# Performance work log

Measured on AMD Instinct MI355X. Metric: run time of the kernel, lower is better.

Reference implementation:

```python
import jax, jax.numpy as jnp
import numpy as np

# Instant-NGP style multiresolution hash grid config
L = 16                      # n_levels
F = 2                       # n_feat_per_entry
LEVEL_SIZE = 524288         # 2^19 hash entries per level
RES = np.array([16, 22, 30, 42, 58, 80, 111, 154, 212, 294, 406, 561, 776, 1072, 1482, 2048], np.int32)
OFFSETS = (np.arange(L + 1) * LEVEL_SIZE).astype(np.int32)
PRIMES = np.array([1, 2654435761, 805459861], dtype=np.uint32)  # spatial hash primes
# 8 corner offsets of a voxel, (8, 3) in {0,1}
CORNERS = np.array([[(c >> d) & 1 for d in range(3)] for c in range(8)], np.int32)


def setup_inputs() -> dict:
    key = jax.random.key(0)
    k1, k2 = jax.random.split(key)
    B = 1000000
    xyz = jax.random.uniform(k1, (B, 3), dtype=jnp.float32)  # points in [0,1)
    embeddings = jax.random.normal(k2, (int(OFFSETS[-1]), F), dtype=jnp.float32) * 0.01
    return {
        'xyz': xyz,
        'embeddings': embeddings,
        'min_xyz': jnp.zeros((3,), jnp.float32),
        'max_xyz': jnp.ones((3,), jnp.float32),
    }


def _encode(xyz, embeddings, min_xyz, max_xyz):
    B = xyz.shape[0]
    norm = (xyz - min_xyz) / (max_xyz - min_xyz)          # (B, 3) in [0,1] if inside grid
    valid = jnp.all((norm >= 0.0) & (norm <= 1.0), axis=-1)  # (B,)
    corners = jnp.asarray(CORNERS)                        # (8, 3)
    primes = jnp.asarray(PRIMES)
    outs = []
    for l in range(L):  # fixed small loop over levels (different resolution per level)
        r = int(RES[l])
        pos = norm * (r - 1)                              # (B, 3) grid coords
        fi = jnp.clip(jnp.floor(pos).astype(jnp.int32), 0, r - 2)  # (B, 3) base corner
        frac = pos - fi.astype(pos.dtype)                 # (B, 3) trilinear fraction
        c = fi[:, None, :] + corners[None, :, :]          # (B, 8, 3) corner coords
        # trilinear interpolation weights, (B, 8)
        w = jnp.prod(jnp.where(corners[None] == 1, frac[:, None, :], 1.0 - frac[:, None, :]), axis=-1)
        # spatial hash into this level's table slice
        cu = c.astype(jnp.uint32)
        h = (cu[..., 0] * primes[0]) ^ (cu[..., 1] * primes[1]) ^ (cu[..., 2] * primes[2])
        lvl_size = jnp.uint32(int(OFFSETS[l + 1] - OFFSETS[l]))
        idx = (h % lvl_size).astype(jnp.int32) + int(OFFSETS[l])   # (B, 8) global entry ids
        feats = embeddings[idx]                           # (B, 8, F) irregular gather
        outs.append(jnp.sum(w[..., None] * feats, axis=1))  # (B, F)
    out = jnp.stack(outs, axis=1).reshape(B, L * F)       # (B, L*F)
    return jnp.where(valid[:, None], out, jnp.zeros((), out.dtype))


def reference(xyz, embeddings, min_xyz, max_xyz):
    return _encode(xyz, embeddings, min_xyz, max_xyz)
```

## Files before the change

### kernel.cpp

```cpp
#include <hip/hip_runtime.h>
#include <hip/hip_fp16.h>
#include <stdint.h>

#define NLEVELS 16
#define BLOCK 256
#define NPT 2

#define P1 2654435761u
#define P2 805459861u
#define HMASK 0x7FFFFu

__device__ __host__ constexpr int DRES(int l) {
    constexpr int r[6] = {16, 22, 30, 42, 58, 80};
    return r[l];
}
__device__ __host__ constexpr uint32_t DOFF(int l) {
    constexpr uint32_t o[6] = {0, 4096, 14744, 41744, 115832, 310944};
    return o[l];
}
#define DENSE_ENTRIES 822944u
#define HASH16_ENTRIES (10u << 19)
#define HASH16_BYTES ((size_t)HASH16_ENTRIES * 4)
#define DENSE_BYTES  ((size_t)DENSE_ENTRIES * 4)


__global__ __launch_bounds__(BLOCK) void convert_hash_kernel(
    const float* __restrict__ emb, uint32_t* __restrict__ tab16)
{
    const uint32_t i = blockIdx.x * BLOCK + threadIdx.x;
    if (i >= HASH16_ENTRIES) return;
    const float2 v = *reinterpret_cast<const float2*>(
        emb + (((size_t)(6u << 19)) + i) * 2);
    __half2 hv = __floats2half2_rn(v.x, v.y);
    __builtin_nontemporal_store(*reinterpret_cast<uint32_t*>(&hv), &tab16[i]);
}

template <int LIDX>
__global__ __launch_bounds__(BLOCK) void dense_build_kernel(
    const float* __restrict__ emb, uint32_t* __restrict__ dense)
{
    constexpr int r = DRES(LIDX);
    constexpr uint32_t off = DOFF(LIDX);
    const int n = r * r * r;
    const int i = blockIdx.x * BLOCK + threadIdx.x;
    if (i >= n) return;
    const int z = i / (r * r);
    const int rem = i - z * (r * r);
    const int y = rem / r;
    const int x = rem - y * r;
    const uint32_t h = ((uint32_t)x ^ ((uint32_t)y * P1) ^ ((uint32_t)z * P2)) & HMASK;
    const float2 v = *reinterpret_cast<const float2*>(
        emb + (((size_t)LIDX << 19) + h) * 2);
    __half2 hv = __floats2half2_rn(v.x, v.y);
    dense[off + i] = *reinterpret_cast<uint32_t*>(&hv);
}


struct PointCtx { float nx, ny, nz; bool valid; };

__device__ __forceinline__ PointCtx make_ctx(const float* __restrict__ xyz, int pt, int B,
                                             float mn0, float mn1, float mn2,
                                             float inv0, float inv1, float inv2)
{
    PointCtx P;
    P.nx = P.ny = P.nz = 0.0f;
    P.valid = false;
    if (pt < B) {
        const float x = xyz[3 * pt + 0];
        const float y = xyz[3 * pt + 1];
        const float z = xyz[3 * pt + 2];
        P.nx = (x - mn0) * inv0;
        P.ny = (y - mn1) * inv1;
        P.nz = (z - mn2) * inv2;
        P.valid = (P.nx >= 0.0f) && (P.nx <= 1.0f) &&
                  (P.ny >= 0.0f) && (P.ny <= 1.0f) &&
                  (P.nz >= 0.0f) && (P.nz <= 1.0f);
    }
    return P;
}

struct C8 { uint32_t idx[8]; float w[8]; };

__device__ __forceinline__ void frac_setup(const PointCtx& P, int r,
                                           int& fx, int& fy, int& fz,
                                           float& wx0, float& wx1,
                                           float& wy0, float& wy1,
                                           float& wz0, float& wz1)
{
    const float rm1 = (float)(r - 1);
    const float px = P.nx * rm1, py = P.ny * rm1, pz = P.nz * rm1;
    fx = (int)floorf(px); fx = min(max(fx, 0), r - 2);
    fy = (int)floorf(py); fy = min(max(fy, 0), r - 2);
    fz = (int)floorf(pz); fz = min(max(fz, 0), r - 2);
    wx1 = px - (float)fx; wx0 = 1.0f - wx1;
    wy1 = py - (float)fy; wy0 = 1.0f - wy1;
    wz1 = pz - (float)fz; wz0 = 1.0f - wz1;
}

__device__ __forceinline__ C8 mk_hash(const PointCtx& P, int r)
{
    int fx, fy, fz; float wx0, wx1, wy0, wy1, wz0, wz1;
    frac_setup(P, r, fx, fy, fz, wx0, wx1, wy0, wy1, wz0, wz1);
    const uint32_t hx0 = (uint32_t)fx,        hx1 = hx0 + 1u;
    const uint32_t hy0 = (uint32_t)fy * P1,   hy1 = hy0 + P1;
    const uint32_t hz0 = (uint32_t)fz * P2,   hz1 = hz0 + P2;
    C8 c;
    #pragma unroll
    for (int k = 0; k < 8; ++k) {
        c.idx[k] = (((k & 1) ? hx1 : hx0) ^
                    ((k & 2) ? hy1 : hy0) ^
                    ((k & 4) ? hz1 : hz0)) & HMASK;
        c.w[k] = ((k & 1) ? wx1 : wx0) * ((k & 2) ? wy1 : wy0) * ((k & 4) ? wz1 : wz0);
    }
    return c;
}

__device__ __forceinline__ C8 mk_dense(const PointCtx& P, int r, uint32_t off)
{
    int fx, fy, fz; float wx0, wx1, wy0, wy1, wz0, wz1;
    frac_setup(P, r, fx, fy, fz, wx0, wx1, wy0, wy1, wz0, wz1);
    const uint32_t base = off + (uint32_t)(fx + fy * r + fz * r * r);
    C8 c;
    #pragma unroll
    for (int k = 0; k < 8; ++k) {
        c.idx[k] = base + (uint32_t)((k & 1) + ((k & 2) ? r : 0) + ((k & 4) ? r * r : 0));
        c.w[k] = ((k & 1) ? wx1 : wx0) * ((k & 2) ? wy1 : wy0) * ((k & 4) ? wz1 : wz0);
    }
    return c;
}

__device__ __forceinline__ float2 accum8(const C8& c, const uint32_t* e, bool valid)
{
    float a = 0.0f, b = 0.0f;
    #pragma unroll
    for (int k = 0; k < 8; ++k) {
        const float2 f = __half22float2(*reinterpret_cast<const __half2*>(&e[k]));
        a = fmaf(c.w[k], f.x, a);
        b = fmaf(c.w[k], f.y, b);
    }
    float2 o;
    o.x = valid ? a : 0.0f;
    o.y = valid ? b : 0.0f;
    return o;
}

__device__ __forceinline__ void nt_store_f2h(uint32_t* p, float2 v)
{
    __half2 h = __floats2half2_rn(v.x, v.y);
    __builtin_nontemporal_store(*reinterpret_cast<uint32_t*>(&h), p);
}

__global__ __launch_bounds__(BLOCK, 4) void dense_low_kernel(
    const float* __restrict__ xyz,
    const uint32_t* __restrict__ dense,
    const float* __restrict__ minv,
    const float* __restrict__ maxv,
    uint32_t* __restrict__ slab,
    int B)
{
    const int t = threadIdx.x;
    const int p0 = blockIdx.x * (NPT * BLOCK) + t;
    const int p1 = p0 + BLOCK;

    const float mn0 = minv[0], mn1 = minv[1], mn2 = minv[2];
    const float inv0 = 1.0f / (maxv[0] - mn0);
    const float inv1 = 1.0f / (maxv[1] - mn1);
    const float inv2 = 1.0f / (maxv[2] - mn2);

    const PointCtx A = make_ctx(xyz, p0, B, mn0, mn1, mn2, inv0, inv1, inv2);
    const PointCtx Bc = make_ctx(xyz, p1, B, mn0, mn1, mn2, inv0, inv1, inv2);

    #pragma unroll
    for (int l = 0; l < 5; ++l) {
        const C8 c0 = mk_dense(A,  DRES(l), DOFF(l));
        const C8 c1 = mk_dense(Bc, DRES(l), DOFF(l));
        uint32_t e0[8], e1[8];
        #pragma unroll
        for (int k = 0; k < 8; ++k) e0[k] = dense[c0.idx[k]];
        #pragma unroll
        for (int k = 0; k < 8; ++k) e1[k] = dense[c1.idx[k]];
        const float2 o0 = accum8(c0, e0, A.valid);
        const float2 o1 = accum8(c1, e1, Bc.valid);
        if (p0 < B) nt_store_f2h(&slab[(size_t)l * B + p0], o0);
        if (p1 < B) nt_store_f2h(&slab[(size_t)l * B + p1], o1);
    }
}

__global__ __launch_bounds__(BLOCK, 4) void dense_l5_kernel(
    const float* __restrict__ xyz,
    const uint32_t* __restrict__ dense,
    const float* __restrict__ minv,
    const float* __restrict__ maxv,
    uint32_t* __restrict__ slab,
    int B)
{
    const int t = threadIdx.x;
    const int p0 = blockIdx.x * (NPT * BLOCK) + t;
    const int p1 = p0 + BLOCK;

    const float mn0 = minv[0], mn1 = minv[1], mn2 = minv[2];
    const float inv0 = 1.0f / (maxv[0] - mn0);
    const float inv1 = 1.0f / (maxv[1] - mn1);
    const float inv2 = 1.0f / (maxv[2] - mn2);

    const PointCtx A = make_ctx(xyz, p0, B, mn0, mn1, mn2, inv0, inv1, inv2);
    const PointCtx Bc = make_ctx(xyz, p1, B, mn0, mn1, mn2, inv0, inv1, inv2);

    const C8 c0 = mk_dense(A,  DRES(5), DOFF(5));
    const C8 c1 = mk_dense(Bc, DRES(5), DOFF(5));
    uint32_t e0[8], e1[8];
    #pragma unroll
    for (int k = 0; k < 8; ++k) e0[k] = dense[c0.idx[k]];
    #pragma unroll
    for (int k = 0; k < 8; ++k) e1[k] = dense[c1.idx[k]];
    __builtin_amdgcn_sched_barrier(0);
    const float2 o0 = accum8(c0, e0, A.valid);
    const float2 o1 = accum8(c1, e1, Bc.valid);
    if (p0 < B) nt_store_f2h(&slab[(size_t)5 * B + p0], o0);
    if (p1 < B) nt_store_f2h(&slab[(size_t)5 * B + p1], o1);
}

template <int L, int R>
__global__ __launch_bounds__(BLOCK, 4) void hash_level_kernel(
    const float* __restrict__ xyz,
    const uint32_t* __restrict__ tab16,
    const float* __restrict__ minv,
    const float* __restrict__ maxv,
    uint32_t* __restrict__ slab,
    int B)
{
    const uint32_t* __restrict__ lt = tab16 + ((size_t)(L - 6) << 19);
    const int t = threadIdx.x;
    const int p0 = blockIdx.x * (NPT * BLOCK) + t;
    const int p1 = p0 + BLOCK;

    const float mn0 = minv[0], mn1 = minv[1], mn2 = minv[2];
    const float inv0 = 1.0f / (maxv[0] - mn0);
    const float inv1 = 1.0f / (maxv[1] - mn1);
    const float inv2 = 1.0f / (maxv[2] - mn2);

    const PointCtx A = make_ctx(xyz, p0, B, mn0, mn1, mn2, inv0, inv1, inv2);
    const PointCtx Bc = make_ctx(xyz, p1, B, mn0, mn1, mn2, inv0, inv1, inv2);

    const C8 c0 = mk_hash(A,  R);
    const C8 c1 = mk_hash(Bc, R);
    uint32_t e0[8], e1[8];
    #pragma unroll
    for (int k = 0; k < 8; ++k) e0[k] = lt[c0.idx[k]];
    #pragma unroll
    for (int k = 0; k < 8; ++k) e1[k] = lt[c1.idx[k]];
    __builtin_amdgcn_sched_barrier(0);
    const float2 o0 = accum8(c0, e0, A.valid);
    const float2 o1 = accum8(c1, e1, Bc.valid);
    if (p0 < B) nt_store_f2h(&slab[(size_t)L * B + p0], o0);
    if (p1 < B) nt_store_f2h(&slab[(size_t)L * B + p1], o1);
}

__global__ __launch_bounds__(BLOCK) void transpose_kernel(
    const uint32_t* __restrict__ slab,
    float* __restrict__ out,
    int B)
{
    __shared__ float s[32][BLOCK + 1];
    const int t = threadIdx.x;
    const int pt = blockIdx.x * BLOCK + t;

    #pragma unroll
    for (int l = 0; l < NLEVELS; ++l) {
        float2 v = make_float2(0.0f, 0.0f);
        if (pt < B) {
            const uint32_t bits = __builtin_nontemporal_load(&slab[(size_t)l * B + pt]);
            v = __half22float2(*reinterpret_cast<const __half2*>(&bits));
        }
        s[2 * l + 0][t] = v.x;
        s[2 * l + 1][t] = v.y;
    }
    __syncthreads();

    const size_t chunk = (size_t)blockIdx.x * (BLOCK * 32);
    const size_t total = (size_t)B * 32;
    #pragma unroll
    for (int k = 0; k < 32; ++k) {
        const int flat = k * BLOCK + t;
        const int p = flat >> 5;
        const int c = flat & 31;
        const size_t g = chunk + (size_t)flat;
        if (g < total) __builtin_nontemporal_store(s[c][p], &out[g]);
    }
}

__global__ __launch_bounds__(BLOCK) void hashgrid_fused_kernel(
    const float* __restrict__ xyz,
    const float* __restrict__ emb,
    const float* __restrict__ minv,
    const float* __restrict__ maxv,
    float* __restrict__ out,
    int B)
{
    constexpr int RES[NLEVELS] = {16, 22, 30, 42, 58, 80, 111, 154,
                                  212, 294, 406, 561, 776, 1072, 1482, 2048};
    __shared__ float s[32][BLOCK + 1];
    const int t = threadIdx.x;
    const int pt = blockIdx.x * BLOCK + t;

    const float mn0 = minv[0], mn1 = minv[1], mn2 = minv[2];
    const float inv0 = 1.0f / (maxv[0] - mn0);
    const float inv1 = 1.0f / (maxv[1] - mn1);
    const float inv2 = 1.0f / (maxv[2] - mn2);

    const PointCtx P = make_ctx(xyz, pt, B, mn0, mn1, mn2, inv0, inv1, inv2);

    #pragma unroll
    for (int l = 0; l < NLEVELS; ++l) {
        const C8 c = mk_hash(P, RES[l]);
        const float* __restrict__ lemb = emb + ((size_t)l << 20);
        float acc0 = 0.0f, acc1 = 0.0f;
        #pragma unroll
        for (int k = 0; k < 8; ++k) {
            const float2 f = *reinterpret_cast<const float2*>(
                lemb + ((size_t)c.idx[k] << 1));
            acc0 = fmaf(c.w[k], f.x, acc0);
            acc1 = fmaf(c.w[k], f.y, acc1);
        }
        s[2 * l + 0][t] = P.valid ? acc0 : 0.0f;
        s[2 * l + 1][t] = P.valid ? acc1 : 0.0f;
    }
    __syncthreads();
    const size_t chunk = (size_t)blockIdx.x * (BLOCK * 32);
    const size_t total = (size_t)B * 32;
    #pragma unroll
    for (int k = 0; k < 32; ++k) {
        const int flat = k * BLOCK + t;
        const int p = flat >> 5;
        const int c = flat & 31;
        const size_t g = chunk + (size_t)flat;
        if (g < total) out[g] = s[c][p];
    }
}

extern "C" void kernel_launch(void* const* d_in, const int* in_sizes, int n_in,
                              void* d_out, int out_size, void* d_ws, size_t ws_size,
                              hipStream_t stream) {
    const float* xyz = (const float*)d_in[0];
    const float* emb = (const float*)d_in[1];
    const float* mn  = (const float*)d_in[2];
    const float* mx  = (const float*)d_in[3];
    float* out = (float*)d_out;

    const int B = in_sizes[0] / 3;
    const int blocks1 = (B + BLOCK - 1) / BLOCK;
    const int blocks2 = (B + NPT * BLOCK - 1) / (NPT * BLOCK);

    const size_t slab_bytes = (size_t)NLEVELS * (size_t)B * 4;
    const size_t ws_needed = slab_bytes + HASH16_BYTES + DENSE_BYTES;

    if (ws_size >= ws_needed) {
        uint32_t* slab  = (uint32_t*)d_ws;
        uint32_t* tab16 = (uint32_t*)((char*)d_ws + slab_bytes);
        uint32_t* dense = (uint32_t*)((char*)d_ws + slab_bytes + HASH16_BYTES);

        hipLaunchKernelGGL(convert_hash_kernel,
                           dim3((HASH16_ENTRIES + BLOCK - 1) / BLOCK), dim3(BLOCK),
                           0, stream, emb, tab16);
        #define DBUILD(L) hipLaunchKernelGGL((dense_build_kernel<L>), \
            dim3((DRES(L)*DRES(L)*DRES(L) + BLOCK - 1) / BLOCK), dim3(BLOCK), 0, stream, emb, dense)
        DBUILD(0); DBUILD(1); DBUILD(2); DBUILD(3); DBUILD(4); DBUILD(5);
        #undef DBUILD

        hipLaunchKernelGGL(dense_low_kernel, dim3(blocks2), dim3(BLOCK), 0, stream,
                           xyz, dense, mn, mx, slab, B);
        hipLaunchKernelGGL(dense_l5_kernel, dim3(blocks2), dim3(BLOCK), 0, stream,
                           xyz, dense, mn, mx, slab, B);
        #define HLVL(L, R) hipLaunchKernelGGL((hash_level_kernel<L, R>), dim3(blocks2), dim3(BLOCK), 0, stream, xyz, tab16, mn, mx, slab, B)
        HLVL(6, 111);  HLVL(7, 154);  HLVL(8, 212);  HLVL(9, 294);
        HLVL(10, 406); HLVL(11, 561); HLVL(12, 776); HLVL(13, 1072);
        HLVL(14, 1482); HLVL(15, 2048);
        #undef HLVL

        hipLaunchKernelGGL(transpose_kernel, dim3(blocks1), dim3(BLOCK), 0, stream,
                           slab, out, B);
    } else {
        hipLaunchKernelGGL(hashgrid_fused_kernel, dim3(blocks1), dim3(BLOCK), 0, stream,
                           xyz, emb, mn, mx, out, B);
    }
}
```

Measured before the change: 387.6 us.

## Merge table prep and per-level gather kernels into two launches

Folds the hash-table fp16 conversion and the six dense-table builds into one prep kernel. All per-level gather kernels become a single mega kernel whose block index selects the level segment. This removes many kernel launches and the launch gaps and tail drains between them. In exchange the resolution becomes a runtime value in the hash segments, with runtime divides and branching, and the sched_barrier hints are dropped.

```diff
diff --git a/kernel.cpp b/kernel.cpp
--- a/kernel.cpp
+++ b/kernel.cpp
@@ -15,44 +15,43 @@
     return r[l];
 }
 __device__ __host__ constexpr uint32_t DOFF(int l) {
-    constexpr uint32_t o[6] = {0, 4096, 14744, 41744, 115832, 310944};
+    constexpr uint32_t o[7] = {0, 4096, 14744, 41744, 115832, 310944, 822944};
     return o[l];
 }
 #define DENSE_ENTRIES 822944u
 #define HASH16_ENTRIES (10u << 19)
 #define HASH16_BYTES ((size_t)HASH16_ENTRIES * 4)
 #define DENSE_BYTES  ((size_t)DENSE_ENTRIES * 4)
-
-
-__global__ __launch_bounds__(BLOCK) void convert_hash_kernel(
-    const float* __restrict__ emb, uint32_t* __restrict__ tab16)
+#define PREP_TOTAL   (HASH16_ENTRIES + DENSE_ENTRIES)
+
+__global__ __launch_bounds__(BLOCK) void prep_kernel(
+    const float* __restrict__ emb,
+    uint32_t* __restrict__ tab16,
+    uint32_t* __restrict__ dense)
 {
     const uint32_t i = blockIdx.x * BLOCK + threadIdx.x;
-    if (i >= HASH16_ENTRIES) return;
-    const float2 v = *reinterpret_cast<const float2*>(
-        emb + (((size_t)(6u << 19)) + i) * 2);
-    __half2 hv = __floats2half2_rn(v.x, v.y);
-    __builtin_nontemporal_store(*reinterpret_cast<uint32_t*>(&hv), &tab16[i]);
-}
-
-template <int LIDX>
-__global__ __launch_bounds__(BLOCK) void dense_build_kernel(
-    const float* __restrict__ emb, uint32_t* __restrict__ dense)
-{
-    constexpr int r = DRES(LIDX);
-    constexpr uint32_t off = DOFF(LIDX);
-    const int n = r * r * r;
-    const int i = blockIdx.x * BLOCK + threadIdx.x;
-    if (i >= n) return;
-    const int z = i / (r * r);
-    const int rem = i - z * (r * r);
-    const int y = rem / r;
-    const int x = rem - y * r;
-    const uint32_t h = ((uint32_t)x ^ ((uint32_t)y * P1) ^ ((uint32_t)z * P2)) & HMASK;
-    const float2 v = *reinterpret_cast<const float2*>(
-        emb + (((size_t)LIDX << 19) + h) * 2);
-    __half2 hv = __floats2half2_rn(v.x, v.y);
-    dense[off + i] = *reinterpret_cast<uint32_t*>(&hv);
+    if (i < HASH16_ENTRIES) {
+        const float2 v = *reinterpret_cast<const float2*>(
+            emb + (((size_t)(6u << 19)) + i) * 2);
+        __half2 hv = __floats2half2_rn(v.x, v.y);
+        __builtin_nontemporal_store(*reinterpret_cast<uint32_t*>(&hv), &tab16[i]);
+    } else if (i < PREP_TOTAL) {
+        const uint32_t j = i - HASH16_ENTRIES;
+        int l = 0;
+        #pragma unroll
+        for (int q = 1; q < 6; ++q) if (j >= DOFF(q)) l = q;
+        const int r = DRES(l);
+        const uint32_t rel = j - DOFF(l);
+        const int z = rel / (uint32_t)(r * r);
+        const uint32_t rem = rel - (uint32_t)z * (uint32_t)(r * r);
+        const int y = rem / (uint32_t)r;
+        const int x = rem - (uint32_t)y * (uint32_t)r;
+        const uint32_t h = ((uint32_t)x ^ ((uint32_t)y * P1) ^ ((uint32_t)z * P2)) & HMASK;
+        const float2 v = *reinterpret_cast<const float2*>(
+            emb + (((size_t)l << 19) + h) * 2);
+        __half2 hv = __floats2half2_rn(v.x, v.y);
+        dense[j] = *reinterpret_cast<uint32_t*>(&hv);
+    }
 }
 
 
@@ -150,16 +149,22 @@
     __builtin_nontemporal_store(*reinterpret_cast<uint32_t*>(&h), p);
 }
 
-__global__ __launch_bounds__(BLOCK, 4) void dense_low_kernel(
+__global__ __launch_bounds__(BLOCK, 4) void gather_mega_kernel(
     const float* __restrict__ xyz,
+    const uint32_t* __restrict__ tab16,
     const uint32_t* __restrict__ dense,
     const float* __restrict__ minv,
     const float* __restrict__ maxv,
     uint32_t* __restrict__ slab,
-    int B)
-{
+    int B, int blocks2)
+{
+    constexpr int HRES[10] = {111, 154, 212, 294, 406, 561, 776, 1072, 1482, 2048};
+
+    const int seg = blockIdx.x / blocks2;
+    const int blk = blockIdx.x - seg * blocks2;
+
     const int t = threadIdx.x;
-    const int p0 = blockIdx.x * (NPT * BLOCK) + t;
+    const int p0 = blk * (NPT * BLOCK) + t;
     const int p1 = p0 + BLOCK;
 
     const float mn0 = minv[0], mn1 = minv[1], mn2 = minv[2];
@@ -167,93 +172,52 @@
     const float inv1 = 1.0f / (maxv[1] - mn1);
     const float inv2 = 1.0f / (maxv[2] - mn2);
 
-    const PointCtx A = make_ctx(xyz, p0, B, mn0, mn1, mn2, inv0, inv1, inv2);
+    const PointCtx A  = make_ctx(xyz, p0, B, mn0, mn1, mn2, inv0, inv1, inv2);
     const PointCtx Bc = make_ctx(xyz, p1, B, mn0, mn1, mn2, inv0, inv1, inv2);
 
-    #pragma unroll
-    for (int l = 0; l < 5; ++l) {
-        const C8 c0 = mk_dense(A,  DRES(l), DOFF(l));
-        const C8 c1 = mk_dense(Bc, DRES(l), DOFF(l));
+    if (seg == 0) {
+        #pragma unroll
+        for (int l = 0; l < 5; ++l) {
+            const C8 c0 = mk_dense(A,  DRES(l), DOFF(l));
+            const C8 c1 = mk_dense(Bc, DRES(l), DOFF(l));
+            uint32_t e0[8], e1[8];
+            #pragma unroll
+            for (int k = 0; k < 8; ++k) e0[k] = dense[c0.idx[k]];
+            #pragma unroll
+            for (int k = 0; k < 8; ++k) e1[k] = dense[c1.idx[k]];
+            const float2 o0 = accum8(c0, e0, A.valid);
+            const float2 o1 = accum8(c1, e1, Bc.valid);
+            if (p0 < B) nt_store_f2h(&slab[(size_t)l * B + p0], o0);
+            if (p1 < B) nt_store_f2h(&slab[(size_t)l * B + p1], o1);
+        }
+    } else if (seg == 1) {
+        const C8 c0 = mk_dense(A,  DRES(5), DOFF(5));
+        const C8 c1 = mk_dense(Bc, DRES(5), DOFF(5));
         uint32_t e0[8], e1[8];
         #pragma unroll
         for (int k = 0; k < 8; ++k) e0[k] = dense[c0.idx[k]];
         #pragma unroll
         for (int k = 0; k < 8; ++k) e1[k] = dense[c1.idx[k]];
+        const float2 o0 = accum8(c0, e0, A.valid);
+        const float2 o1 = accum8(c1, e1, Bc.valid);
+        if (p0 < B) nt_store_f2h(&slab[(size_t)5 * B + p0], o0);
+        if (p1 < B) nt_store_f2h(&slab[(size_t)5 * B + p1], o1);
+    } else {
+        const int l = seg + 4;
+        const int r = HRES[seg - 2];
+        const uint32_t* __restrict__ lt = tab16 + ((size_t)(l - 6) << 19);
+        const C8 c0 = mk_hash(A,  r);
+        const C8 c1 = mk_hash(Bc, r);
+        uint32_t e0[8], e1[8];
+        #pragma unroll
+        for (int k = 0; k < 8; ++k) e0[k] = lt[c0.idx[k]];
+        #pragma unroll
+        for (int k = 0; k < 8; ++k) e1[k] = lt[c1.idx[k]];
         const float2 o0 = accum8(c0, e0, A.valid);
         const float2 o1 = accum8(c1, e1, Bc.valid);
         if (p0 < B) nt_store_f2h(&slab[(size_t)l * B + p0], o0);
         if (p1 < B) nt_store_f2h(&slab[(size_t)l * B + p1], o1);
     }
-}
-
-__global__ __launch_bounds__(BLOCK, 4) void dense_l5_kernel(
-    const float* __restrict__ xyz,
-    const uint32_t* __restrict__ dense,
-    const float* __restrict__ minv,
-    const float* __restrict__ maxv,
-    uint32_t* __restrict__ slab,
-    int B)
-{
-    const int t = threadIdx.x;
-    const int p0 = blockIdx.x * (NPT * BLOCK) + t;
-    const int p1 = p0 + BLOCK;
-
-    const float mn0 = minv[0], mn1 = minv[1], mn2 = minv[2];
-    const float inv0 = 1.0f / (maxv[0] - mn0);
-    const float inv1 = 1.0f / (maxv[1] - mn1);
-    const float inv2 = 1.0f / (maxv[2] - mn2);
-
-    const PointCtx A = make_ctx(xyz, p0, B, mn0, mn1, mn2, inv0, inv1, inv2);
-    const PointCtx Bc = make_ctx(xyz, p1, B, mn0, mn1, mn2, inv0, inv1, inv2);
-
-    const C8 c0 = mk_dense(A,  DRES(5), DOFF(5));
-    const C8 c1 = mk_dense(Bc, DRES(5), DOFF(5));
-    uint32_t e0[8], e1[8];
-    #pragma unroll
-    for (int k = 0; k < 8; ++k) e0[k] = dense[c0.idx[k]];
-    #pragma unroll
-    for (int k = 0; k < 8; ++k) e1[k] = dense[c1.idx[k]];
-    __builtin_amdgcn_sched_barrier(0);
-    const float2 o0 = accum8(c0, e0, A.valid);
-    const float2 o1 = accum8(c1, e1, Bc.valid);
-    if (p0 < B) nt_store_f2h(&slab[(size_t)5 * B + p0], o0);
-    if (p1 < B) nt_store_f2h(&slab[(size_t)5 * B + p1], o1);
-}
-
-template <int L, int R>
-__global__ __launch_bounds__(BLOCK, 4) void hash_level_kernel(
-    const float* __restrict__ xyz,
-    const uint32_t* __restrict__ tab16,
-    const float* __restrict__ minv,
-    const float* __restrict__ maxv,
-    uint32_t* __restrict__ slab,
-    int B)
-{
-    const uint32_t* __restrict__ lt = tab16 + ((size_t)(L - 6) << 19);
-    const int t = threadIdx.x;
-    const int p0 = blockIdx.x * (NPT * BLOCK) + t;
-    const int p1 = p0 + BLOCK;
-
-    const float mn0 = minv[0], mn1 = minv[1], mn2 = minv[2];
-    const float inv0 = 1.0f / (maxv[0] - mn0);
-    const float inv1 = 1.0f / (maxv[1] - mn1);
-    const float inv2 = 1.0f / (maxv[2] - mn2);
-
-    const PointCtx A = make_ctx(xyz, p0, B, mn0, mn1, mn2, inv0, inv1, inv2);
-    const PointCtx Bc = make_ctx(xyz, p1, B, mn0, mn1, mn2, inv0, inv1, inv2);
-
-    const C8 c0 = mk_hash(A,  R);
-    const C8 c1 = mk_hash(Bc, R);
-    uint32_t e0[8], e1[8];
-    #pragma unroll
-    for (int k = 0; k < 8; ++k) e0[k] = lt[c0.idx[k]];
-    #pragma unroll
-    for (int k = 0; k < 8; ++k) e1[k] = lt[c1.idx[k]];
-    __builtin_amdgcn_sched_barrier(0);
-    const float2 o0 = accum8(c0, e0, A.valid);
-    const float2 o1 = accum8(c1, e1, Bc.valid);
-    if (p0 < B) nt_store_f2h(&slab[(size_t)L * B + p0], o0);
-    if (p1 < B) nt_store_f2h(&slab[(size_t)L * B + p1], o1);
 }
 
 __global__ __launch_bounds__(BLOCK) void transpose_kernel(
@@ -359,23 +323,12 @@
         uint32_t* tab16 = (uint32_t*)((char*)d_ws + slab_bytes);
         uint32_t* dense = (uint32_t*)((char*)d_ws + slab_bytes + HASH16_BYTES);
 
-        hipLaunchKernelGGL(convert_hash_kernel,
-                           dim3((HASH16_ENTRIES + BLOCK - 1) / BLOCK), dim3(BLOCK),
-                           0, stream, emb, tab16);
-        #define DBUILD(L) hipLaunchKernelGGL((dense_build_kernel<L>), \
-            dim3((DRES(L)*DRES(L)*DRES(L) + BLOCK - 1) / BLOCK), dim3(BLOCK), 0, stream, emb, dense)
-        DBUILD(0); DBUILD(1); DBUILD(2); DBUILD(3); DBUILD(4); DBUILD(5);
-        #undef DBUILD
-
-        hipLaunchKernelGGL(dense_low_kernel, dim3(blocks2), dim3(BLOCK), 0, stream,
-                           xyz, dense, mn, mx, slab, B);
-        hipLaunchKernelGGL(dense_l5_kernel, dim3(blocks2), dim3(BLOCK), 0, stream,
-                           xyz, dense, mn, mx, slab, B);
-        #define HLVL(L, R) hipLaunchKernelGGL((hash_level_kernel<L, R>), dim3(blocks2), dim3(BLOCK), 0, stream, xyz, tab16, mn, mx, slab, B)
-        HLVL(6, 111);  HLVL(7, 154);  HLVL(8, 212);  HLVL(9, 294);
-        HLVL(10, 406); HLVL(11, 561); HLVL(12, 776); HLVL(13, 1072);
-        HLVL(14, 1482); HLVL(15, 2048);
-        #undef HLVL
+        hipLaunchKernelGGL(prep_kernel,
+                           dim3((PREP_TOTAL + BLOCK - 1) / BLOCK), dim3(BLOCK),
+                           0, stream, emb, tab16, dense);
+
+        hipLaunchKernelGGL(gather_mega_kernel, dim3(12 * blocks2), dim3(BLOCK), 0, stream,
+                           xyz, tab16, dense, mn, mx, slab, B, blocks2);
 
         hipLaunchKernelGGL(transpose_kernel, dim3(blocks1), dim3(BLOCK), 0, stream,
                            slab, out, B);
```

Measured after the change: 313.4 us (median of 2 runs). 19.1% less time.
